# Kernel optimization log

Measured on AMD Instinct MI355X. Metric: run time of the kernel, lower is better.

Reference implementation:

```python
import jax, jax.numpy as jnp
import numpy as np

B, L, H, V = 2048, 1024, 64, 64
LN_EPS = 1e-5
DELTA_EPS = 1e-6


def setup_inputs() -> dict:
    key = jax.random.key(0)
    ks = jax.random.split(key, 16)
    s = 0.05
    return {
        'seq': jax.random.randint(ks[0], (B, L), 0, V),
        'embed_W': jax.random.normal(ks[1], (V, H), jnp.float32),
        'ff_w1': jax.random.normal(ks[2], (H, 2 * H), jnp.float32) * s,
        'ff_b1': jnp.zeros((2 * H,), jnp.float32),
        'ff_w2': jax.random.normal(ks[3], (2 * H, H), jnp.float32) * s,
        'ff_b2': jnp.zeros((H,), jnp.float32),
        'ln_g': jnp.ones((H,), jnp.float32),
        'ln_b': jnp.zeros((H,), jnp.float32),
        'gate_w1': jax.random.normal(ks[4], (H, 16), jnp.float32) * s,
        'gate_b1': jnp.zeros((16,), jnp.float32),
        'gate_w2': jax.random.normal(ks[5], (16, 1), jnp.float32) * s,
        'gate_b2': jnp.zeros((1,), jnp.float32),
        'read_w': jax.random.normal(ks[6], (H, H), jnp.float32) * s,
        'read_b': jnp.zeros((H,), jnp.float32),
        'out_w': jax.random.normal(ks[7], (H, V), jnp.float32) * s,
        'out_b': jnp.zeros((V,), jnp.float32),
    }


def _layernorm(x, g, b):
    mu = jnp.mean(x, axis=-1, keepdims=True)
    var = jnp.var(x, axis=-1, keepdims=True)
    return (x - mu) * jax.lax.rsqrt(var + LN_EPS) * g + b


def reference(seq, embed_W, ff_w1, ff_b1, ff_w2, ff_b2, ln_g, ln_b,
              gate_w1, gate_b1, gate_w2, gate_b2, read_w, read_b, out_w, out_b):
    h = embed_W[seq]                                        # (B, L, H)
    ff = jnp.maximum(h @ ff_w1 + ff_b1, 0.0) @ ff_w2 + ff_b2
    h = _layernorm(h + ff, ln_g, ln_b)                      # (B, L, H)

    ks_seq = jnp.transpose(h[:, :-1, :], (1, 0, 2))         # (L-1, B, H) keys for scan

    def step(M, k):
        # k: (B, H); M: (B, H, H) fast-weight memory
        g = jax.nn.sigmoid(jnp.maximum(k @ gate_w1 + gate_b1, 0.0) @ gate_w2 + gate_b2)  # (B, 1)
        v_pred = jnp.einsum('bij,bj->bi', jax.lax.stop_gradient(M), k)
        denom = jnp.sum(k * k, axis=-1, keepdims=True) + DELTA_EPS
        dv = k - v_pred / denom                             # (B, H)
        dM = dv[:, :, None] * k[:, None, :]                 # outer product (B, H, H)
        return M + g[:, :, None] * dM, None

    M0 = jnp.zeros((h.shape[0], H, H), h.dtype)
    M, _ = jax.lax.scan(step, M0, ks_seq)

    q = h[:, -1, :]
    ctx = jnp.einsum('bij,bj->bi', M, q)                    # (B, H)
    logits = (ctx @ read_w + read_b) @ out_w + out_b        # (B, V)
    return logits
```

## Files before the change

kernel.cpp:

```cpp
#include <hip/hip_runtime.h>
#include <math.h>

#define Bsz 2048
#define Lsz 1024
#define SW  8

#define OFF_G   0
#define OFF_GC  4096
#define OFF_P   8192
#define OFF_WC  12288
#define OFF_GV  16384
#define OFF_C   16448
#define OFF_BC  16512

__device__ __forceinline__ float __rlf(float v, int i) {
    return __int_as_float(__builtin_amdgcn_readlane(__float_as_int(v), i));
}

__global__ __launch_bounds__(128) void prep1_kernel(
    const float* __restrict__ embed_W, const float* __restrict__ ff_w1, const float* __restrict__ ff_b1,
    const float* __restrict__ ff_w2, const float* __restrict__ ff_b2, const float* __restrict__ ln_g,
    const float* __restrict__ ln_b, const float* __restrict__ gate_w1, const float* __restrict__ gate_b1,
    const float* __restrict__ gate_w2, const float* __restrict__ gate_b2, const float* __restrict__ read_w,
    const float* __restrict__ read_b, const float* __restrict__ out_w, const float* __restrict__ out_b,
    float* __restrict__ ws)
{
    const int tid = threadIdx.x;
    const int blk = blockIdx.x;
    if (blk < 64) {
        const int v = blk;
        __shared__ float z[128];
        __shared__ float hsh[64];
        const float* Ev = embed_W + (v << 6);
        float a = ff_b1[tid];
        #pragma unroll
        for (int i = 0; i < 64; ++i) a = fmaf(Ev[i], ff_w1[i * 128 + tid], a);
        z[tid] = fmaxf(a, 0.0f);
        __syncthreads();
        if (tid < 64) {
            float x = Ev[tid] + ff_b2[tid];
            #pragma unroll
            for (int j = 0; j < 128; ++j) x = fmaf(z[j], ff_w2[j * 64 + tid], x);
            float mu = x;
            #pragma unroll
            for (int off = 32; off > 0; off >>= 1) mu += __shfl_xor(mu, off);
            mu *= (1.0f / 64.0f);
            const float dd = x - mu;
            float var = dd * dd;
            #pragma unroll
            for (int off = 32; off > 0; off >>= 1) var += __shfl_xor(var, off);
            var *= (1.0f / 64.0f);
            const float rstd = rsqrtf(var + 1e-5f);
            const float hv = fmaf(dd * rstd, ln_g[tid], ln_b[tid]);
            hsh[tid] = hv;
            float dn = hv * hv;
            #pragma unroll
            for (int off = 32; off > 0; off >>= 1) dn += __shfl_xor(dn, off);
            dn += 1e-6f;
            float a2 = 0.0f;
            if (tid < 16) {
                float um = gate_b1[tid];
                #pragma unroll
                for (int i = 0; i < 64; ++i) um = fmaf(hsh[i], gate_w1[i * 16 + tid], um);
                a2 = fmaxf(um, 0.0f) * gate_w2[tid];
            }
            #pragma unroll
            for (int off = 8; off > 0; off >>= 1) a2 += __shfl_xor(a2, off);
            ws[OFF_G + (v << 6) + tid] = hv;
            if (tid == 0) {
                a2 += gate_b2[0];
                const float g = 1.0f / (1.0f + expf(-a2));
                ws[OFF_GV + v] = g;
                ws[OFF_C + v]  = g / dn;
            }
        }
    } else if (blk < 128) {
        const int j = blk - 64;
        if (tid < 64) {
            float a = 0.0f;
            #pragma unroll
            for (int m = 0; m < 64; ++m) a = fmaf(read_w[(j << 6) + m], out_w[(m << 6) + tid], a);
            ws[OFF_WC + (j << 6) + tid] = a;
        }
    } else {
        if (tid < 64) {
            float a = out_b[tid];
            #pragma unroll
            for (int jj = 0; jj < 64; ++jj) a = fmaf(read_b[jj], out_w[(jj << 6) + tid], a);
            ws[OFF_BC + tid] = a;
        }
    }
}

__global__ __launch_bounds__(64) void prep2_kernel(float* __restrict__ ws)
{
    const int tid = threadIdx.x;
    const int blk = blockIdx.x;
    __shared__ float tT[65 * 64];
    for (int idx = tid; idx < 4096; idx += 64) {
        const int w = idx >> 6, j = idx & 63;
        tT[j * 65 + w] = ws[OFF_G + idx];
    }
    __syncthreads();
    if (blk < 64) {
        const int v = blk;
        const float cv = ws[OFF_C + v];
        float a = 0.0f;
        #pragma unroll
        for (int j = 0; j < 64; ++j) a = fmaf(tT[j * 65 + v], tT[j * 65 + tid], a);
        ws[OFF_G  + (v << 6) + tid] = a;
        ws[OFF_GC + (v << 6) + tid] = cv * a;
    } else {
        const int v = blk - 64;
        const float gv = ws[OFF_GV + v];
        float a = 0.0f;
        #pragma unroll
        for (int j = 0; j < 64; ++j)
            a = fmaf(tT[j * 65 + v], ws[OFF_WC + (j << 6) + tid], a);
        ws[OFF_P + (v << 6) + tid] = gv * a;
    }
}

__global__ __launch_bounds__(SW * 64) void scan_kernel(const int* __restrict__ seq,
                                                       const float* __restrict__ ws,
                                                       float* __restrict__ out)
{
    __shared__ float2 ldsGP[65 * 64];
    __shared__ int    pk[SW][16 + 256 + 64];
    __shared__ float  ldsbc[64];

    const int tid  = threadIdx.x;
    const int wave = tid >> 6;
    const int lane = tid & 63;

    {
        const float4* srcGc = (const float4*)(ws + OFF_GC);
        const float4* srcP  = (const float4*)(ws + OFF_P);
        for (int i = tid; i < 1024; i += SW * 64) {
            const float4 g4 = srcGc[i];
            const float4 p4 = srcP[i];
            const int base = i << 2;
            ldsGP[base + 0] = make_float2(g4.x, p4.x);
            ldsGP[base + 1] = make_float2(g4.y, p4.y);
            ldsGP[base + 2] = make_float2(g4.z, p4.z);
            ldsGP[base + 3] = make_float2(g4.w, p4.w);
        }
    }
    if (tid < 64) {
        ldsGP[4096 + tid] = make_float2(0.0f, 0.0f);
        ldsbc[tid] = ws[OFF_BC + tid];
    }
    const int b = blockIdx.x * SW + wave;
    int* P = pk[wave] + 16;
    {
        const int4* src = (const int4*)(seq + (size_t)b * Lsz);
        #pragma unroll
        for (int i = 0; i < 4; ++i) {
            const int4 tv = src[i * 64 + lane];
            P[i * 64 + lane] = tv.x | (tv.y << 8) | (tv.z << 16) | (tv.w << 24);
        }
        if (lane < 16) pk[wave][lane] = 0x40404040;
    }
    __syncthreads();

    const int lastw = P[255];
    const int tokL  = (lastw >> 24) & 0xFF;
    if (lane == 0) P[255] = (lastw & 0x00FFFFFF) | (64 << 24);

    float D   = ws[OFF_G + (tokL << 6) + lane];
    float acc = ldsbc[lane];

    int    tkA[16], tkB[16];
    float2 gpA[16], gpB[16];

    int tokv = P[248 + lane];
    #pragma unroll
    for (int j = 0; j < 4; ++j) {
        const int w = __builtin_amdgcn_readlane(tokv, 7 - j);
        tkA[4 * j + 0] = (w >> 24) & 0xFF;
        tkA[4 * j + 1] = (w >> 16) & 0xFF;
        tkA[4 * j + 2] = (w >>  8) & 0xFF;
        tkA[4 * j + 3] =  w        & 0xFF;
    }
    #pragma unroll
    for (int k = 0; k < 16; ++k) gpA[k] = ldsGP[(tkA[k] << 6) + lane];

    for (int t0 = 1023; t0 > 0; t0 -= 32) {
        const int tokvN = P[(((t0 - 32) >> 2) - 7) + lane];
        #pragma unroll
        for (int j = 0; j < 4; ++j) {
            const int w = __builtin_amdgcn_readlane(tokv, 3 - j);
            tkB[4 * j + 0] = (w >> 24) & 0xFF;
            tkB[4 * j + 1] = (w >> 16) & 0xFF;
            tkB[4 * j + 2] = (w >>  8) & 0xFF;
            tkB[4 * j + 3] =  w        & 0xFF;
        }
        #pragma unroll
        for (int k = 0; k < 16; ++k) gpB[k] = ldsGP[(tkB[k] << 6) + lane];
        #pragma unroll
        for (int k = 0; k < 16; ++k) {
            const float d = __rlf(D, tkA[k]);
            D   = fmaf(-d, gpA[k].x, D);
            acc = fmaf( d, gpA[k].y, acc);
        }
        #pragma unroll
        for (int j = 0; j < 4; ++j) {
            const int w = __builtin_amdgcn_readlane(tokvN, 7 - j);
            tkA[4 * j + 0] = (w >> 24) & 0xFF;
            tkA[4 * j + 1] = (w >> 16) & 0xFF;
            tkA[4 * j + 2] = (w >>  8) & 0xFF;
            tkA[4 * j + 3] =  w        & 0xFF;
        }
        #pragma unroll
        for (int k = 0; k < 16; ++k) gpA[k] = ldsGP[(tkA[k] << 6) + lane];
        #pragma unroll
        for (int k = 0; k < 16; ++k) {
            const float d = __rlf(D, tkB[k]);
            D   = fmaf(-d, gpB[k].x, D);
            acc = fmaf( d, gpB[k].y, acc);
        }
        tokv = tokvN;
    }

    out[(size_t)b * 64 + lane] = acc;
}

extern "C" void kernel_launch(void* const* d_in, const int* in_sizes, int n_in,
                              void* d_out, int out_size, void* d_ws, size_t ws_size,
                              hipStream_t stream) {
    const int*   seq     = (const int*)  d_in[0];
    const float* embed_W = (const float*)d_in[1];
    const float* ff_w1   = (const float*)d_in[2];
    const float* ff_b1   = (const float*)d_in[3];
    const float* ff_w2   = (const float*)d_in[4];
    const float* ff_b2   = (const float*)d_in[5];
    const float* ln_g    = (const float*)d_in[6];
    const float* ln_b    = (const float*)d_in[7];
    const float* gate_w1 = (const float*)d_in[8];
    const float* gate_b1 = (const float*)d_in[9];
    const float* gate_w2 = (const float*)d_in[10];
    const float* gate_b2 = (const float*)d_in[11];
    const float* read_w  = (const float*)d_in[12];
    const float* read_b  = (const float*)d_in[13];
    const float* out_w   = (const float*)d_in[14];
    const float* out_b   = (const float*)d_in[15];
    float* ws  = (float*)d_ws;
    float* out = (float*)d_out;

    hipLaunchKernelGGL(prep1_kernel, dim3(129), dim3(128), 0, stream,
                       embed_W, ff_w1, ff_b1, ff_w2, ff_b2, ln_g, ln_b,
                       gate_w1, gate_b1, gate_w2, gate_b2, read_w, read_b,
                       out_w, out_b, ws);
    hipLaunchKernelGGL(prep2_kernel, dim3(128), dim3(64), 0, stream, ws);
    hipLaunchKernelGGL(scan_kernel, dim3(Bsz / SW), dim3(SW * 64), 0, stream,
                       seq, ws, out);
}
```

Measured before the change: 123.2 us.

## Pack two batch rows per wavefront with two hidden dims per lane

Each wavefront now processes two batch elements: each half of the wave handles one sequence, and each lane holds two hidden dimensions, with G and P interleaved into float4 LDS entries. Tokens are read straight from global memory per step instead of being packed into bytes in LDS first. The goal is to halve the wave count and fetch twice the table data per LDS read. The cost is four readlanes per token instead of one, extra selects, and many scalar or global token loads inside the loop.

```diff
diff --git a/kernel.cpp b/kernel.cpp
--- a/kernel.cpp
+++ b/kernel.cpp
@@ -3,7 +3,6 @@
 
 #define Bsz 2048
 #define Lsz 1024
-#define SW  8
 
 #define OFF_G   0
 #define OFF_GC  4096
@@ -121,108 +120,113 @@
     }
 }
 
-__global__ __launch_bounds__(SW * 64) void scan_kernel(const int* __restrict__ seq,
-                                                       const float* __restrict__ ws,
-                                                       float* __restrict__ out)
+__global__ __launch_bounds__(256) void scan_kernel(const int* __restrict__ seq,
+                                                   const float* __restrict__ ws,
+                                                   float* __restrict__ out)
 {
-    __shared__ float2 ldsGP[65 * 64];
-    __shared__ int    pk[SW][16 + 256 + 64];
-    __shared__ float  ldsbc[64];
+    __shared__ float4 ldsGP4[65 * 32];
 
     const int tid  = threadIdx.x;
     const int wave = tid >> 6;
     const int lane = tid & 63;
+    const int m    = lane & 31;
+    const bool hi  = lane >= 32;
 
     {
         const float4* srcGc = (const float4*)(ws + OFF_GC);
         const float4* srcP  = (const float4*)(ws + OFF_P);
-        for (int i = tid; i < 1024; i += SW * 64) {
+        for (int i = tid; i < 1024; i += 256) {
+            const int v = i >> 4, q = i & 15;
             const float4 g4 = srcGc[i];
             const float4 p4 = srcP[i];
-            const int base = i << 2;
-            ldsGP[base + 0] = make_float2(g4.x, p4.x);
-            ldsGP[base + 1] = make_float2(g4.y, p4.y);
-            ldsGP[base + 2] = make_float2(g4.z, p4.z);
-            ldsGP[base + 3] = make_float2(g4.w, p4.w);
-        }
-    }
-    if (tid < 64) {
-        ldsGP[4096 + tid] = make_float2(0.0f, 0.0f);
-        ldsbc[tid] = ws[OFF_BC + tid];
-    }
-    const int b = blockIdx.x * SW + wave;
-    int* P = pk[wave] + 16;
+            ldsGP4[v * 32 + 2 * q]     = make_float4(g4.x, p4.x, g4.y, p4.y);
+            ldsGP4[v * 32 + 2 * q + 1] = make_float4(g4.z, p4.z, g4.w, p4.w);
+        }
+        if (tid < 32) ldsGP4[2048 + tid] = make_float4(0.f, 0.f, 0.f, 0.f);
+    }
+    __syncthreads();
+
+    const int gw = blockIdx.x * 4 + wave;
+    const int b0 = gw << 1, b1 = b0 + 1;
+    const int* sp0 = seq + (size_t)b0 * Lsz;
+    const int* sp1 = seq + (size_t)b1 * Lsz;
+
+    const int tL0 = sp0[1023], tL1 = sp1[1023];
+    const int tL  = hi ? tL1 : tL0;
+    const float2 gi  = *(const float2*)(ws + OFF_G  + (tL << 6) + (m << 1));
+    const float2 bc2 = *(const float2*)(ws + OFF_BC + (m << 1));
+    float De = gi.x, Do = gi.y;
+    float ae = bc2.x, ao = bc2.y;
+
+    int    tkA0[16], tkA1[16], tkB0[16], tkB1[16];
+    float4 gpA[16], gpB[16];
+
     {
-        const int4* src = (const int4*)(seq + (size_t)b * Lsz);
-        #pragma unroll
-        for (int i = 0; i < 4; ++i) {
-            const int4 tv = src[i * 64 + lane];
-            P[i * 64 + lane] = tv.x | (tv.y << 8) | (tv.z << 16) | (tv.w << 24);
-        }
-        if (lane < 16) pk[wave][lane] = 0x40404040;
-    }
-    __syncthreads();
-
-    const int lastw = P[255];
-    const int tokL  = (lastw >> 24) & 0xFF;
-    if (lane == 0) P[255] = (lastw & 0x00FFFFFF) | (64 << 24);
-
-    float D   = ws[OFF_G + (tokL << 6) + lane];
-    float acc = ldsbc[lane];
-
-    int    tkA[16], tkB[16];
-    float2 gpA[16], gpB[16];
-
-    int tokv = P[248 + lane];
-    #pragma unroll
-    for (int j = 0; j < 4; ++j) {
-        const int w = __builtin_amdgcn_readlane(tokv, 7 - j);
-        tkA[4 * j + 0] = (w >> 24) & 0xFF;
-        tkA[4 * j + 1] = (w >> 16) & 0xFF;
-        tkA[4 * j + 2] = (w >>  8) & 0xFF;
-        tkA[4 * j + 3] =  w        & 0xFF;
-    }
-    #pragma unroll
-    for (int k = 0; k < 16; ++k) gpA[k] = ldsGP[(tkA[k] << 6) + lane];
-
-    for (int t0 = 1023; t0 > 0; t0 -= 32) {
-        const int tokvN = P[(((t0 - 32) >> 2) - 7) + lane];
-        #pragma unroll
-        for (int j = 0; j < 4; ++j) {
-            const int w = __builtin_amdgcn_readlane(tokv, 3 - j);
-            tkB[4 * j + 0] = (w >> 24) & 0xFF;
-            tkB[4 * j + 1] = (w >> 16) & 0xFF;
-            tkB[4 * j + 2] = (w >>  8) & 0xFF;
-            tkB[4 * j + 3] =  w        & 0xFF;
-        }
-        #pragma unroll
-        for (int k = 0; k < 16; ++k) gpB[k] = ldsGP[(tkB[k] << 6) + lane];
+        const int base = 1008;
+        #pragma unroll
+        for (int k = 0; k < 16; ++k) { tkA0[k] = sp0[base + 15 - k]; tkA1[k] = sp1[base + 15 - k]; }
+        tkA0[0] = 64; tkA1[0] = 64;
         #pragma unroll
         for (int k = 0; k < 16; ++k) {
-            const float d = __rlf(D, tkA[k]);
-            D   = fmaf(-d, gpA[k].x, D);
-            acc = fmaf( d, gpA[k].y, acc);
-        }
-        #pragma unroll
-        for (int j = 0; j < 4; ++j) {
-            const int w = __builtin_amdgcn_readlane(tokvN, 7 - j);
-            tkA[4 * j + 0] = (w >> 24) & 0xFF;
-            tkA[4 * j + 1] = (w >> 16) & 0xFF;
-            tkA[4 * j + 2] = (w >>  8) & 0xFF;
-            tkA[4 * j + 3] =  w        & 0xFF;
-        }
-        #pragma unroll
-        for (int k = 0; k < 16; ++k) gpA[k] = ldsGP[(tkA[k] << 6) + lane];
+            const int t = hi ? tkA1[k] : tkA0[k];
+            gpA[k] = ldsGP4[(t << 5) + m];
+        }
+    }
+
+    for (int h = 0; h < 64; h += 2) {
+        {
+            const int base = 1008 - ((h + 1) << 4);
+            #pragma unroll
+            for (int k = 0; k < 16; ++k) { tkB0[k] = sp0[base + 15 - k]; tkB1[k] = sp1[base + 15 - k]; }
+            #pragma unroll
+            for (int k = 0; k < 16; ++k) {
+                const int t = hi ? tkB1[k] : tkB0[k];
+                gpB[k] = ldsGP4[(t << 5) + m];
+            }
+        }
         #pragma unroll
         for (int k = 0; k < 16; ++k) {
-            const float d = __rlf(D, tkB[k]);
-            D   = fmaf(-d, gpB[k].x, D);
-            acc = fmaf( d, gpB[k].y, acc);
-        }
-        tokv = tokvN;
-    }
-
-    out[(size_t)b * 64 + lane] = acc;
+            const int t0 = tkA0[k], t1 = tkA1[k];
+            const float e0 = __rlf(De, t0 >> 1),        o0 = __rlf(Do, t0 >> 1);
+            const float e1 = __rlf(De, 32 + (t1 >> 1)), o1 = __rlf(Do, 32 + (t1 >> 1));
+            const float d0 = (t0 & 1) ? o0 : e0;
+            const float d1 = (t1 & 1) ? o1 : e1;
+            const float vd = hi ? d1 : d0;
+            const float4 gp = gpA[k];
+            De = fmaf(-vd, gp.x, De);
+            Do = fmaf(-vd, gp.z, Do);
+            ae = fmaf( vd, gp.y, ae);
+            ao = fmaf( vd, gp.w, ao);
+        }
+        {
+            int base = 1008 - ((h + 2) << 4);
+            if (base < 0) base = 0;
+            #pragma unroll
+            for (int k = 0; k < 16; ++k) { tkA0[k] = sp0[base + 15 - k]; tkA1[k] = sp1[base + 15 - k]; }
+            #pragma unroll
+            for (int k = 0; k < 16; ++k) {
+                const int t = hi ? tkA1[k] : tkA0[k];
+                gpA[k] = ldsGP4[(t << 5) + m];
+            }
+        }
+        #pragma unroll
+        for (int k = 0; k < 16; ++k) {
+            const int t0 = tkB0[k], t1 = tkB1[k];
+            const float e0 = __rlf(De, t0 >> 1),        o0 = __rlf(Do, t0 >> 1);
+            const float e1 = __rlf(De, 32 + (t1 >> 1)), o1 = __rlf(Do, 32 + (t1 >> 1));
+            const float d0 = (t0 & 1) ? o0 : e0;
+            const float d1 = (t1 & 1) ? o1 : e1;
+            const float vd = hi ? d1 : d0;
+            const float4 gp = gpB[k];
+            De = fmaf(-vd, gp.x, De);
+            Do = fmaf(-vd, gp.z, Do);
+            ae = fmaf( vd, gp.y, ae);
+            ao = fmaf( vd, gp.w, ao);
+        }
+    }
+
+    const int b = hi ? b1 : b0;
+    *(float2*)(out + (size_t)b * 64 + (m << 1)) = make_float2(ae, ao);
 }
 
 extern "C" void kernel_launch(void* const* d_in, const int* in_sizes, int n_in,
@@ -252,6 +256,6 @@
                        gate_w1, gate_b1, gate_w2, gate_b2, read_w, read_b,
                        out_w, out_b, ws);
     hipLaunchKernelGGL(prep2_kernel, dim3(128), dim3(64), 0, stream, ws);
-    hipLaunchKernelGGL(scan_kernel, dim3(Bsz / SW), dim3(SW * 64), 0, stream,
+    hipLaunchKernelGGL(scan_kernel, dim3(Bsz / 8), dim3(256), 0, stream,
                        seq, ws, out);
 }
```

Measured after the change: 161.4 us. +31.1%, slower.
